# Optimization experiments

Hardware: AMD Instinct MI355X
Metric: run time of the kernel (lower is better)

The kernel has to match this reference:

```python
import jax, jax.numpy as jnp
import numpy as np

D_MODEL = 1024
NUM_HEADS = 16
D_K = D_MODEL // NUM_HEADS
SCALE = float(np.sqrt(D_K))


def setup_inputs() -> dict:
    key = jax.random.key(0)
    ks = jax.random.split(key, 12)
    B, S = 4, 2048
    s = 1.0 / np.sqrt(D_MODEL)
    inp = {
        'query': jax.random.normal(ks[0], (B, S, D_MODEL), jnp.float32),
        'key':   jax.random.normal(ks[1], (B, S, D_MODEL), jnp.float32),
        'value': jax.random.normal(ks[2], (B, S, D_MODEL), jnp.float32),
        'Wq': jax.random.normal(ks[3], (D_MODEL, D_MODEL), jnp.float32) * s,
        'bq': jax.random.normal(ks[4], (D_MODEL,), jnp.float32) * s,
        'Wk': jax.random.normal(ks[5], (D_MODEL, D_MODEL), jnp.float32) * s,
        'bk': jax.random.normal(ks[6], (D_MODEL,), jnp.float32) * s,
        'Wv': jax.random.normal(ks[7], (D_MODEL, D_MODEL), jnp.float32) * s,
        'bv': jax.random.normal(ks[8], (D_MODEL,), jnp.float32) * s,
        'Wo': jax.random.normal(ks[9], (D_MODEL, D_MODEL), jnp.float32) * s,
        'bo': jax.random.normal(ks[10], (D_MODEL,), jnp.float32) * s,
    }
    return inp


def reference(query, key, value, Wq, bq, Wk, bk, Wv, bv, Wo, bo):
    B, Sq, _ = query.shape
    Skv = key.shape[1]
    # torch Linear: x @ W.T + b
    def proj(x, W, b, S):
        y = jnp.einsum('bsd,ed->bse', x, W) + b
        return y.reshape(B, S, NUM_HEADS, D_K).transpose(0, 2, 1, 3)  # [B,H,S,dk]
    Q = proj(query, Wq, bq, Sq)
    K = proj(key, Wk, bk, Skv)
    V = proj(value, Wv, bv, Skv)
    scores = jnp.einsum('bhqd,bhkd->bhqk', Q, K) / SCALE  # [B,H,Sq,Skv]
    attn = jax.nn.softmax(scores, axis=-1)  # dropout=0 -> identity
    out = jnp.einsum('bhqk,bhkd->bhqd', attn, V)
    out = out.transpose(0, 2, 1, 3).reshape(B, Sq, D_MODEL)
    out = jnp.einsum('bsd,ed->bse', out, Wo) + bo
    return out
```

## Files before the change

### kernel.cpp

```cpp
#include <hip/hip_runtime.h>


typedef __attribute__((ext_vector_type(8))) __bf16 bf16x8;
typedef __attribute__((ext_vector_type(4))) __bf16 bf16x4;
typedef __attribute__((ext_vector_type(4))) float f32x4;
typedef __attribute__((ext_vector_type(4))) short s16x4;

#define SCALE_FOLD 0.18033688011112043f

__device__ __forceinline__ void async_copy16(const void* g, void* lds) {
  __builtin_amdgcn_global_load_lds(
      (const __attribute__((address_space(1))) void*)g,
      (__attribute__((address_space(3))) void*)lds, 16, 0, 0);
}

template <int ROWS, int THREADS>
__device__ __forceinline__ void stage_tile(const __bf16* __restrict__ g, int ld,
                                           __bf16* lds, int tid) {
  const int wave_base = tid & ~63;
#pragma unroll
  for (int r = 0; r < ROWS * 8 / THREADS; ++r) {
    int slot = r * THREADS + tid;
    int row = slot >> 3;
    int c = slot & 7;
    int gc = c ^ (row & 7);
    async_copy16(g + row * ld + gc * 8, lds + (r * THREADS + wave_base) * 8);
  }
}

__device__ __forceinline__ bf16x8 frag_ld(const __bf16* lds, int row, int chunk) {
  return *(const bf16x8*)(lds + row * 64 + ((chunk ^ (row & 7)) << 3));
}

__global__ void cvt_all(const float* __restrict__ s0, const float* __restrict__ s1,
                        const float* __restrict__ s2, const float* __restrict__ s3,
                        const float* __restrict__ s4, const float* __restrict__ s5,
                        const float* __restrict__ s6, __bf16* d0, __bf16* d1,
                        __bf16* d2, __bf16* d3, __bf16* d4, __bf16* d5,
                        __bf16* d6, int n4_big, int n4_small) {
  const int z = blockIdx.y;
  const float* src;
  __bf16* dst;
  int n4;
  switch (z) {
    case 0: src = s0; dst = d0; n4 = n4_big; break;
    case 1: src = s1; dst = d1; n4 = n4_big; break;
    case 2: src = s2; dst = d2; n4 = n4_big; break;
    case 3: src = s3; dst = d3; n4 = n4_small; break;
    case 4: src = s4; dst = d4; n4 = n4_small; break;
    case 5: src = s5; dst = d5; n4 = n4_small; break;
    default: src = s6; dst = d6; n4 = n4_small; break;
  }
  int i = blockIdx.x * blockDim.x + threadIdx.x;
  if (i < n4) {
    float4 v = ((const float4*)src)[i];
    bf16x4 o = {(__bf16)v.x, (__bf16)v.y, (__bf16)v.z, (__bf16)v.w};
    ((bf16x4*)dst)[i] = o;
  }
}

__device__ __forceinline__ void gemm_body(const __bf16* __restrict__ A,
                                          const __bf16* __restrict__ B,
                                          const float* __restrict__ bias,
                                          void* __restrict__ out, int K,
                                          int mode, int m0, int n0,
                                          __bf16* Alds, __bf16* Blds) {
  const int tid = threadIdx.x;
  const int lane = tid & 63;
  const int w = tid >> 6;
  const int wm = w >> 1, wn = w & 1;
  const int l15 = lane & 15, quad = lane >> 4;

  f32x4 acc[4][4] = {};

  for (int k0 = 0; k0 < K; k0 += 64) {
    stage_tile<128, 256>(A + m0 * K + k0, K, Alds, tid);
    stage_tile<128, 256>(B + n0 * K + k0, K, Blds, tid);
    __syncthreads();
#pragma unroll
    for (int kc = 0; kc < 2; ++kc) {
      bf16x8 af[4], bfr[4];
#pragma unroll
      for (int mi = 0; mi < 4; ++mi)
        af[mi] = frag_ld(Alds, wm * 64 + mi * 16 + l15, kc * 4 + quad);
#pragma unroll
      for (int ni = 0; ni < 4; ++ni)
        bfr[ni] = frag_ld(Blds, wn * 64 + ni * 16 + l15, kc * 4 + quad);
#pragma unroll
      for (int mi = 0; mi < 4; ++mi)
#pragma unroll
        for (int ni = 0; ni < 4; ++ni)
          acc[mi][ni] = __builtin_amdgcn_mfma_f32_16x16x32_bf16(
              af[mi], bfr[ni], acc[mi][ni], 0, 0, 0);
    }
    __syncthreads();
  }

#pragma unroll
  for (int mi = 0; mi < 4; ++mi) {
#pragma unroll
    for (int i = 0; i < 4; ++i) {
      int grow = m0 + wm * 64 + mi * 16 + quad * 4 + i;
#pragma unroll
      for (int ni = 0; ni < 4; ++ni) {
        int gcol = n0 + wn * 64 + ni * 16 + l15;
        float v = acc[mi][ni][i];
        if (mode == 3) {
          v += bias[gcol];
          ((float*)out)[grow * 1024 + gcol] = v;
        } else if (mode == 2) {
          v += bias[grow];
          int h = grow >> 6, dd = grow & 63;
          int b = gcol >> 11, s = gcol & 2047;
          ((__bf16*)out)[(((b * 16 + h) * 64 + dd) * 2048) + s] = (__bf16)v;
        } else {
          v += bias[gcol];
          if (mode == 0) v *= SCALE_FOLD;
          int h = gcol >> 6, dd = gcol & 63;
          int b = grow >> 11, s = grow & 2047;
          ((__bf16*)out)[(((b * 16 + h) * 2048 + s) * 64) + dd] = (__bf16)v;
        }
      }
    }
  }
}

__device__ __forceinline__ void remap_xcd(int lid, int& mblk, int& nblk) {
  int xcd = lid & 7;
  int j = lid >> 3;
  mblk = xcd * 8 + (j >> 3);
  nblk = j & 7;
}

__global__ __launch_bounds__(256) void gemm_qkv(
    const __bf16* __restrict__ xq, const __bf16* __restrict__ xk,
    const __bf16* __restrict__ xv, const __bf16* __restrict__ wq,
    const __bf16* __restrict__ wk, const __bf16* __restrict__ wv,
    const float* __restrict__ bq, const float* __restrict__ bk,
    const float* __restrict__ bv, __bf16* Qb, __bf16* Kb, __bf16* Vtb) {
  __shared__ alignas(16) __bf16 Alds[128 * 64];
  __shared__ alignas(16) __bf16 Blds[128 * 64];
  int mblk, nblk;
  remap_xcd(blockIdx.x, mblk, nblk);
  const int z = blockIdx.y;
  if (z == 0) {
    gemm_body(xq, wq, bq, Qb, 1024, 0, mblk * 128, nblk * 128, Alds, Blds);
  } else if (z == 1) {
    gemm_body(xk, wk, bk, Kb, 1024, 1, mblk * 128, nblk * 128, Alds, Blds);
  } else {
    gemm_body(wv, xv, bv, Vtb, 1024, 2, nblk * 128, mblk * 128, Alds, Blds);
  }
}

__global__ __launch_bounds__(256) void gemm_out(const __bf16* __restrict__ A,
                                                const __bf16* __restrict__ B,
                                                const float* __restrict__ bias,
                                                float* __restrict__ out) {
  __shared__ alignas(16) __bf16 Alds[128 * 64];
  __shared__ alignas(16) __bf16 Blds[128 * 64];
  int mblk, nblk;
  remap_xcd(blockIdx.x, mblk, nblk);
  gemm_body(A, B, bias, out, 1024, 3, mblk * 128, nblk * 128, Alds, Blds);
}

__global__ __launch_bounds__(128, 2) void attn_kernel(
    const __bf16* __restrict__ Qg, const __bf16* __restrict__ Kg,
    const __bf16* __restrict__ Vt, __bf16* __restrict__ AO) {
  __shared__ alignas(16) __bf16 Klds[2][64 * 64];
  __shared__ alignas(16) __bf16 Vlds[2][64 * 64];

  const int tid = threadIdx.x;
  const int lane = tid & 63;
  const int w = tid >> 6;
  const int l15 = lane & 15, quad = lane >> 4;
  const int S = 2048;

  const int bid = blockIdx.x;
  const int r = bid >> 3;
  const int bh = (bid & 7) * 8 + (r & 7);
  const int q0 = (r >> 3) * 128;

  const __bf16* Qbase = Qg + (size_t)bh * S * 64;
  const __bf16* Kbase = Kg + (size_t)bh * S * 64;
  const __bf16* Vbase = Vt + (size_t)bh * 64 * S;

  stage_tile<128, 128>(Qbase + q0 * 64, 64, (__bf16*)Klds, tid);
  __syncthreads();
  bf16x8 qf[4][2];
#pragma unroll
  for (int qi = 0; qi < 4; ++qi)
#pragma unroll
    for (int kc = 0; kc < 2; ++kc)
      qf[qi][kc] =
          frag_ld((__bf16*)Klds, w * 64 + qi * 16 + l15, kc * 4 + quad);
  __syncthreads();

  stage_tile<64, 128>(Kbase, 64, Klds[0], tid);
  stage_tile<64, 128>(Vbase, S, Vlds[0], tid);
  __syncthreads();

  const s16x4 ones = {0x3F80, 0x3F80, 0x3F80, 0x3F80};

  f32x4 oacc[4][4] = {};
  f32x4 lacc[4] = {};

  for (int mt = 0; mt < 32; ++mt) {
    const int cur = mt & 1;
    if (mt + 1 < 32) {
      stage_tile<64, 128>(Kbase + (mt + 1) * 64 * 64, 64, Klds[cur ^ 1], tid);
      stage_tile<64, 128>(Vbase + (mt + 1) * 64, S, Vlds[cur ^ 1], tid);
    }

    f32x4 sacc[4][4] = {};
#pragma unroll
    for (int kc = 0; kc < 2; ++kc) {
      bf16x8 kf[4];
#pragma unroll
      for (int ci = 0; ci < 4; ++ci)
        kf[ci] = frag_ld(Klds[cur], ci * 16 + l15, kc * 4 + quad);
#pragma unroll
      for (int ci = 0; ci < 4; ++ci)
#pragma unroll
        for (int qi = 0; qi < 4; ++qi)
          sacc[ci][qi] = __builtin_amdgcn_mfma_f32_16x16x32_bf16(
              kf[ci], qf[qi][kc], sacc[ci][qi], 0, 0, 0);
    }

#pragma unroll
    for (int ci = 0; ci < 4; ++ci) {
      s16x4 vfs[4];
#pragma unroll
      for (int ni = 0; ni < 4; ++ni) {
        int row = ni * 16 + l15;
        int c0 = ci * 16 + quad * 4;
        int addr = row * 64 + (((c0 >> 3) ^ (row & 7)) << 3) + (c0 & 7);
        vfs[ni] = *(const s16x4*)(Vlds[cur] + addr);
      }
#pragma unroll
      for (int qi = 0; qi < 4; ++qi) {
        bf16x4 pk;
#pragma unroll
        for (int i = 0; i < 4; ++i)
          pk[i] = (__bf16)__builtin_amdgcn_exp2f(sacc[ci][qi][i]);
        s16x4 pks = __builtin_bit_cast(s16x4, pk);
        lacc[qi] = __builtin_amdgcn_mfma_f32_16x16x16bf16_1k(pks, ones,
                                                             lacc[qi], 0, 0, 0);
#pragma unroll
        for (int ni = 0; ni < 4; ++ni)
          oacc[qi][ni] = __builtin_amdgcn_mfma_f32_16x16x16bf16_1k(
              pks, vfs[ni], oacc[qi][ni], 0, 0, 0);
      }
    }
    __syncthreads();
  }

  const int b = bh >> 4;
  const int hh = bh & 15;
#pragma unroll
  for (int qi = 0; qi < 4; ++qi) {
#pragma unroll
    for (int i = 0; i < 4; ++i) {
      int s = q0 + w * 64 + qi * 16 + quad * 4 + i;
      float inv_l = 1.f / lacc[qi][i];
#pragma unroll
      for (int ni = 0; ni < 4; ++ni) {
        int d = ni * 16 + l15;
        AO[((size_t)(b * 2048 + s)) * 1024 + hh * 64 + d] =
            (__bf16)(oacc[qi][ni][i] * inv_l);
      }
    }
  }
}

extern "C" void kernel_launch(void* const* d_in, const int* in_sizes, int n_in,
                              void* d_out, int out_size, void* d_ws,
                              size_t ws_size, hipStream_t stream) {
  const float* q_in = (const float*)d_in[0];
  const float* k_in = (const float*)d_in[1];
  const float* v_in = (const float*)d_in[2];
  const float* Wq = (const float*)d_in[3];
  const float* bq = (const float*)d_in[4];
  const float* Wk = (const float*)d_in[5];
  const float* bk = (const float*)d_in[6];
  const float* Wv = (const float*)d_in[7];
  const float* bv = (const float*)d_in[8];
  const float* Wo = (const float*)d_in[9];
  const float* bo = (const float*)d_in[10];

  const size_t SZ_X = (size_t)8192 * 1024 * 2;
  const size_t SZ_W = (size_t)1024 * 1024 * 2;
  char* p = (char*)d_ws;
  __bf16* xq = (__bf16*)p; p += SZ_X;
  __bf16* xk = (__bf16*)p; p += SZ_X;
  __bf16* xv = (__bf16*)p; p += SZ_X;
  __bf16* wqb = (__bf16*)p; p += SZ_W;
  __bf16* wkb = (__bf16*)p; p += SZ_W;
  __bf16* wvb = (__bf16*)p; p += SZ_W;
  __bf16* wob = (__bf16*)p; p += SZ_W;
  __bf16* Qb = (__bf16*)p; p += SZ_X;
  __bf16* Kb = (__bf16*)p; p += SZ_X;
  __bf16* Vtb = (__bf16*)p; p += SZ_X;
  __bf16* AOb = (__bf16*)p; p += SZ_X;

  const int nx4 = 8192 * 1024 / 4, nw4 = 1024 * 1024 / 4;
  cvt_all<<<dim3(nx4 / 256, 7), 256, 0, stream>>>(
      q_in, k_in, v_in, Wq, Wk, Wv, Wo, xq, xk, xv, wqb, wkb, wvb, wob, nx4,
      nw4);

  gemm_qkv<<<dim3(512, 3), 256, 0, stream>>>(xq, xk, xv, wqb, wkb, wvb, bq,
                                             bk, bv, Qb, Kb, Vtb);

  attn_kernel<<<1024, 128, 0, stream>>>(Qb, Kb, Vtb, AOb);

  gemm_out<<<512, 256, 0, stream>>>(AOb, wob, bo, (float*)d_out);
}
```

Baseline: 337.4 us.

## Use 16x16x32 MFMA for PV via permlane-swapped P fragments and setprio

Replaces the 16x16x16 bf16 MFMAs for the P·V and row-sum products with 16x16x32 MFMAs. This halves the MFMA instruction count and lets V fragments load as 16-byte swizzled reads instead of 8-byte ones. The P accumulator layout is turned into the K=32 operand layout with v_permlane32/16_swap instructions on packed bf16 pairs. It also raises wave priority around the MFMA blocks with s_setprio, to favour matrix issue over other waves. The cost is extra permlane ops, and correctness depends on the lane permutation matching the V fragment ordering.

```diff
diff --git a/kernel.cpp b/kernel.cpp
--- a/kernel.cpp
+++ b/kernel.cpp
@@ -4,7 +4,7 @@
 typedef __attribute__((ext_vector_type(8))) __bf16 bf16x8;
 typedef __attribute__((ext_vector_type(4))) __bf16 bf16x4;
 typedef __attribute__((ext_vector_type(4))) float f32x4;
-typedef __attribute__((ext_vector_type(4))) short s16x4;
+typedef __attribute__((ext_vector_type(4))) unsigned int u32x4;
 
 #define SCALE_FOLD 0.18033688011112043f
 
@@ -30,6 +30,12 @@
 
 __device__ __forceinline__ bf16x8 frag_ld(const __bf16* lds, int row, int chunk) {
   return *(const bf16x8*)(lds + row * 64 + ((chunk ^ (row & 7)) << 3));
+}
+
+__device__ __forceinline__ unsigned pk_bf16(float lo, float hi) {
+  unsigned short l = __builtin_bit_cast(unsigned short, (__bf16)lo);
+  unsigned short h = __builtin_bit_cast(unsigned short, (__bf16)hi);
+  return (unsigned)l | ((unsigned)h << 16);
 }
 
 __global__ void cvt_all(const float* __restrict__ s0, const float* __restrict__ s1,
@@ -199,7 +205,8 @@
   stage_tile<64, 128>(Vbase, S, Vlds[0], tid);
   __syncthreads();
 
-  const s16x4 ones = {0x3F80, 0x3F80, 0x3F80, 0x3F80};
+  const u32x4 ones_u = {0x3F803F80u, 0x3F803F80u, 0x3F803F80u, 0x3F803F80u};
+  const bf16x8 ones8 = __builtin_bit_cast(bf16x8, ones_u);
 
   f32x4 oacc[4][4] = {};
   f32x4 lacc[4] = {};
@@ -218,37 +225,48 @@
 #pragma unroll
       for (int ci = 0; ci < 4; ++ci)
         kf[ci] = frag_ld(Klds[cur], ci * 16 + l15, kc * 4 + quad);
+      __builtin_amdgcn_s_setprio(1);
 #pragma unroll
       for (int ci = 0; ci < 4; ++ci)
 #pragma unroll
         for (int qi = 0; qi < 4; ++qi)
           sacc[ci][qi] = __builtin_amdgcn_mfma_f32_16x16x32_bf16(
               kf[ci], qf[qi][kc], sacc[ci][qi], 0, 0, 0);
-    }
-
-#pragma unroll
-    for (int ci = 0; ci < 4; ++ci) {
-      s16x4 vfs[4];
-#pragma unroll
-      for (int ni = 0; ni < 4; ++ni) {
-        int row = ni * 16 + l15;
-        int c0 = ci * 16 + quad * 4;
-        int addr = row * 64 + (((c0 >> 3) ^ (row & 7)) << 3) + (c0 & 7);
-        vfs[ni] = *(const s16x4*)(Vlds[cur] + addr);
-      }
+      __builtin_amdgcn_s_setprio(0);
+    }
+
+#pragma unroll
+    for (int t = 0; t < 2; ++t) {
+      bf16x8 vf[4];
+#pragma unroll
+      for (int ni = 0; ni < 4; ++ni)
+        vf[ni] = frag_ld(Vlds[cur], ni * 16 + l15, t * 4 + quad);
 #pragma unroll
       for (int qi = 0; qi < 4; ++qi) {
-        bf16x4 pk;
-#pragma unroll
-        for (int i = 0; i < 4; ++i)
-          pk[i] = (__bf16)__builtin_amdgcn_exp2f(sacc[ci][qi][i]);
-        s16x4 pks = __builtin_bit_cast(s16x4, pk);
-        lacc[qi] = __builtin_amdgcn_mfma_f32_16x16x16bf16_1k(pks, ones,
-                                                             lacc[qi], 0, 0, 0);
+        float ea[4], eb[4];
+#pragma unroll
+        for (int i = 0; i < 4; ++i) {
+          ea[i] = __builtin_amdgcn_exp2f(sacc[2 * t][qi][i]);
+          eb[i] = __builtin_amdgcn_exp2f(sacc[2 * t + 1][qi][i]);
+        }
+        unsigned a0 = pk_bf16(ea[0], ea[1]);
+        unsigned a1 = pk_bf16(ea[2], ea[3]);
+        unsigned b0 = pk_bf16(eb[0], eb[1]);
+        unsigned b1 = pk_bf16(eb[2], eb[3]);
+        asm("v_permlane32_swap_b32 %0, %1" : "+v"(a0), "+v"(b0));
+        asm("v_permlane16_swap_b32 %0, %1" : "+v"(a0), "+v"(b0));
+        asm("v_permlane32_swap_b32 %0, %1" : "+v"(a1), "+v"(b1));
+        asm("v_permlane16_swap_b32 %0, %1" : "+v"(a1), "+v"(b1));
+        u32x4 pw = {a0, a1, b0, b1};
+        bf16x8 pf = __builtin_bit_cast(bf16x8, pw);
+        __builtin_amdgcn_s_setprio(1);
+        lacc[qi] = __builtin_amdgcn_mfma_f32_16x16x32_bf16(pf, ones8, lacc[qi],
+                                                           0, 0, 0);
 #pragma unroll
         for (int ni = 0; ni < 4; ++ni)
-          oacc[qi][ni] = __builtin_amdgcn_mfma_f32_16x16x16bf16_1k(
-              pks, vfs[ni], oacc[qi][ni], 0, 0, 0);
+          oacc[qi][ni] = __builtin_amdgcn_mfma_f32_16x16x32_bf16(
+              pf, vf[ni], oacc[qi][ni], 0, 0, 0);
+        __builtin_amdgcn_s_setprio(0);
       }
     }
     __syncthreads();
```

Result: no change. 337.1 us (-0.1%).
